# Performance work log

Measured on AMD Instinct MI355X. Metric: run time of the kernel, lower is better.

## Reference

```python
import jax, jax.numpy as jnp
import numpy as np

EPS = 1e-8
INV_SQRT = 1.0 / np.sqrt(1.0 + EPS)  # 1/sqrt(|k|+eps), |k|=1 for both hyp and sph


def layernorm(x, w, b, eps=1e-5):
    m = jnp.mean(x, axis=-1, keepdims=True)
    v = jnp.mean((x - m) ** 2, axis=-1, keepdims=True)
    return (x - m) * jax.lax.rsqrt(v + eps) * w + b


def setup_inputs() -> dict:
    key = jax.random.key(0)
    B, S, D, H = 4, 1024, 512, 8
    d = D // H
    FF = 2048
    ks = jax.random.split(key, 12)
    s_attn = 1.0 / np.sqrt(d)
    s_d = 1.0 / np.sqrt(D)
    s_ff = 1.0 / np.sqrt(FF)
    return {
        "x": jax.random.normal(ks[0], (B, S, D), jnp.float32),
        "Wq": jax.random.normal(ks[1], (H, d, d), jnp.float32) * s_attn,
        "Wk": jax.random.normal(ks[2], (H, d, d), jnp.float32) * s_attn,
        "Wv": jax.random.normal(ks[3], (H, d, d), jnp.float32) * s_attn,
        "gw": jnp.ones((H, 3), jnp.float32) / 3.0,
        "temp": jnp.ones((H,), jnp.float32),
        "Wo": jax.random.normal(ks[4], (D, D), jnp.float32) * s_d,
        "bo": jnp.zeros((D,), jnp.float32),
        "ln1_w": jnp.ones((D,), jnp.float32),
        "ln1_b": jnp.zeros((D,), jnp.float32),
        "ln2_w": jnp.ones((D,), jnp.float32),
        "ln2_b": jnp.zeros((D,), jnp.float32),
        "W1": jax.random.normal(ks[5], (FF, D), jnp.float32) * s_d,
        "b1": jnp.zeros((FF,), jnp.float32),
        "W2": jax.random.normal(ks[6], (D, FF), jnp.float32) * s_ff,
        "b2": jnp.zeros((D,), jnp.float32),
    }


def reference(x, Wq, Wk, Wv, gw, temp, Wo, bo, ln1_w, ln1_b, ln2_w, ln2_b, W1, b1, W2, b2):
    B, S, D = x.shape
    H = Wq.shape[0]
    d = D // H

    h = layernorm(x, ln1_w, ln1_b)
    xh = h.reshape(B, S, H, d).transpose(0, 2, 1, 3)  # [B,H,S,d]
    # nn.Linear: y = x @ W^T
    q = jnp.einsum("bhsd,hed->bhse", xh, Wq)
    k = jnp.einsum("bhsd,hed->bhse", xh, Wk)
    v = jnp.einsum("bhsd,hed->bhse", xh, Wv)

    qsq = jnp.sum(q * q, axis=-1)  # [B,H,S] == ||q||^2
    ksq = jnp.sum(k * k, axis=-1)
    qk = jnp.einsum("bhsd,bhtd->bhst", q, k)
    # ||q-k||^2 via expansion (same math as sum(diff^2), avoids [B,H,S,S,d])
    dsq = jnp.maximum(qsq[..., :, None] + ksq[..., None, :] - 2.0 * qk, 0.0)
    euc = jnp.sqrt(dsq + EPS)

    denom = (1.0 - qsq)[..., :, None] * (1.0 - ksq)[..., None, :] + EPS
    cosh_arg = jnp.clip(1.0 + 2.0 * dsq / denom, 1.0, 1e6)
    hyp = jnp.arccosh(cosh_arg) * INV_SQRT

    qn = jnp.sqrt(qsq)
    kn = jnp.sqrt(ksq)
    cos_angle = qk / ((qn + EPS)[..., :, None] * (kn + EPS)[..., None, :])
    cos_angle = jnp.clip(cos_angle, -1.0 + EPS, 1.0 - EPS)
    sph = jnp.arccos(cos_angle) * INV_SQRT

    w = jax.nn.softmax(gw, axis=-1)  # [H,3] per-head geometry mixing
    comb = (
        w[:, 0, None, None] * hyp
        + w[:, 1, None, None] * euc
        + w[:, 2, None, None] * sph
    )
    sim = -comb * temp[None, :, None, None]
    attn = jax.nn.softmax(sim, axis=-1)
    out = jnp.einsum("bhst,bhtd->bhsd", attn, v)
    out = out.transpose(0, 2, 1, 3).reshape(B, S, D)
    attn_out = out @ Wo.T + bo

    x = x + attn_out  # dropout=0 (eval)
    h2 = layernorm(x, ln2_w, ln2_b)
    ff = jax.nn.gelu(h2 @ W1.T + b1, approximate=False) @ W2.T + b2
    return x + ff, w
```

## Files before the change

### kernel.cpp

```cpp
#include <hip/hip_runtime.h>
#include <hip/hip_bf16.h>
#include <math.h>

typedef __attribute__((ext_vector_type(4))) float f32x4;
typedef __attribute__((ext_vector_type(8))) short bf16x8;
typedef unsigned short u16;
typedef unsigned int u32;

typedef f32x4  __attribute__((may_alias)) f32x4a;
typedef bf16x8 __attribute__((may_alias)) bf16x8a;
typedef uint2  __attribute__((may_alias)) uint2a;

__device__ __forceinline__ u16 bfbits(float f) {
  union { __hip_bfloat16 h; u16 u; } cv;
  cv.h = __float2bfloat16(f);
  return cv.u;
}
__device__ __forceinline__ float rcp_r(float x)  { return __builtin_amdgcn_rcpf(x); }
__device__ __forceinline__ float sqrt_r(float x) { return __builtin_amdgcn_sqrtf(x); }
__device__ __forceinline__ float log2_r(float x) { return __builtin_amdgcn_logf(x); }
__device__ __forceinline__ float exp2_r(float x) { return __builtin_amdgcn_exp2f(x); }
__device__ __forceinline__ u32 cvt_pk_bf16(float lo, float hi) {
  u32 r;
  asm("v_cvt_pk_bf16_f32 %0, %1, %2" : "=v"(r) : "v"(lo), "v"(hi));
  return r;
}
typedef const __attribute__((address_space(1))) unsigned int* gas_t;
typedef __attribute__((address_space(3))) unsigned int* las_t;
__device__ __forceinline__ void gload_lds16(const u16* g, u16* l) {
  __builtin_amdgcn_global_load_lds((gas_t)g, (las_t)l, 16, 0, 0);
}

__global__ __launch_bounds__(256) void convert_weights(
    const float* __restrict__ wq, const float* __restrict__ wk, const float* __restrict__ wv,
    const float* __restrict__ wo, const float* __restrict__ w1, const float* __restrict__ w2,
    u16* __restrict__ owq, u16* __restrict__ owk, u16* __restrict__ owv,
    u16* __restrict__ owo, u16* __restrict__ ow1, u16* __restrict__ ow2) {
  int i = blockIdx.x * 256 + threadIdx.x;
  const float* src; u16* dst; int base;
  if (i < 8192)        { src = wq; dst = owq; base = 0; }
  else if (i < 16384)  { src = wk; dst = owk; base = 8192; }
  else if (i < 24576)  { src = wv; dst = owv; base = 16384; }
  else if (i < 90112)  { src = wo; dst = owo; base = 24576; }
  else if (i < 352256) { src = w1; dst = ow1; base = 90112; }
  else                 { src = w2; dst = ow2; base = 352256; }
  int li = i - base;
  float4 v = reinterpret_cast<const float4*>(src)[li];
  ushort4 o;
  o.x = bfbits(v.x); o.y = bfbits(v.y); o.z = bfbits(v.z); o.w = bfbits(v.w);
  reinterpret_cast<ushort4*>(dst)[li] = o;
}

__global__ __launch_bounds__(128) void ln_kernel(const float* __restrict__ x,
    const float* __restrict__ w, const float* __restrict__ b, u16* __restrict__ out) {
  int row = blockIdx.x, tid = threadIdx.x;
  float4 v = reinterpret_cast<const float4*>(x + row * 512)[tid];
  float s  = v.x + v.y + v.z + v.w;
  float s2 = v.x*v.x + v.y*v.y + v.z*v.z + v.w*v.w;
  #pragma unroll
  for (int o = 32; o > 0; o >>= 1) { s += __shfl_down(s, o); s2 += __shfl_down(s2, o); }
  __shared__ float sm[4];
  if ((tid & 63) == 0) { sm[(tid >> 6)*2] = s; sm[(tid >> 6)*2 + 1] = s2; }
  __syncthreads();
  float ts = sm[0] + sm[2], ts2 = sm[1] + sm[3];
  float mean = ts * (1.f/512.f);
  float var  = ts2 * (1.f/512.f) - mean*mean;
  float rstd = __builtin_amdgcn_rsqf(var + 1e-5f);
  float4 wv = reinterpret_cast<const float4*>(w)[tid];
  float4 bv = reinterpret_cast<const float4*>(b)[tid];
  ushort4 o;
  o.x = bfbits((v.x-mean)*rstd*wv.x + bv.x);
  o.y = bfbits((v.y-mean)*rstd*wv.y + bv.y);
  o.z = bfbits((v.z-mean)*rstd*wv.z + bv.z);
  o.w = bfbits((v.w-mean)*rstd*wv.w + bv.w);
  reinterpret_cast<ushort4*>(out + row * 512)[tid] = o;
}

__global__ __launch_bounds__(256) void qkv_kernel(const u16* __restrict__ h1,
    const u16* __restrict__ wqb, const u16* __restrict__ wkb, const u16* __restrict__ wvb,
    u16* __restrict__ q, u16* __restrict__ k, u16* __restrict__ vt,
    float* __restrict__ qsq, float* __restrict__ ksq) {
  int mt = blockIdx.x, head = blockIdx.y;
  int wave = threadIdx.x >> 6, lane = threadIdx.x & 63;
  int lr = lane & 15, lg = lane >> 4;
  int m0 = mt * 64 + wave * 16;
  const u16* xr = h1 + (m0 + lr) * 512 + head * 64 + lg * 8;
  bf16x8 a0 = *reinterpret_cast<const bf16x8a*>(xr);
  bf16x8 a1 = *reinterpret_cast<const bf16x8a*>(xr + 32);
  int m_base = m0 + 4*lg;
  int bq = m_base >> 10;
  int s_base = m_base & 1023;
  int bh = (bq << 3) + head;
  #pragma unroll 1
  for (int mat = 0; mat < 3; ++mat) {
    const u16* W = (mat == 0 ? wqb : mat == 1 ? wkb : wvb) + head * 4096;
    f32x4 acc[4];
    #pragma unroll
    for (int c = 0; c < 4; c++)
      #pragma unroll
      for (int j = 0; j < 4; j++) acc[c][j] = 0.f;
    #pragma unroll
    for (int c = 0; c < 4; c++) {
      const u16* wr = W + (c*16 + lr) * 64 + lg * 8;
      bf16x8 b0 = *reinterpret_cast<const bf16x8a*>(wr);
      bf16x8 b1 = *reinterpret_cast<const bf16x8a*>(wr + 32);
      acc[c] = __builtin_amdgcn_mfma_f32_16x16x32_bf16(a0, b0, acc[c], 0, 0, 0);
      acc[c] = __builtin_amdgcn_mfma_f32_16x16x32_bf16(a1, b1, acc[c], 0, 0, 0);
    }
    if (mat == 2) {
      #pragma unroll
      for (int c = 0; c < 4; c++)
        #pragma unroll
        for (int j = 0; j < 4; j++)
          vt[(bh*64 + c*16 + lr) * 1024 + s_base + j] = bfbits(acc[c][j]);
    } else {
      u16* dst = (mat == 0 ? q : k);
      float* sq = (mat == 0 ? qsq : ksq);
      float ss[4] = {0.f, 0.f, 0.f, 0.f};
      #pragma unroll
      for (int c = 0; c < 4; c++)
        #pragma unroll
        for (int j = 0; j < 4; j++) {
          float vv = acc[c][j];
          dst[(bh*1024 + s_base + j) * 64 + c*16 + lr] = bfbits(vv);
          ss[j] += vv * vv;
        }
      #pragma unroll
      for (int j = 0; j < 4; j++) {
        #pragma unroll
        for (int o = 1; o < 16; o <<= 1) ss[j] += __shfl_xor(ss[j], o);
      }
      if (lr == 0) {
        #pragma unroll
        for (int j = 0; j < 4; j++) sq[bh*1024 + s_base + j] = ss[j];
      }
    }
  }
}

__global__ __launch_bounds__(512) void attn_kernel(
    const u16* __restrict__ q, const u16* __restrict__ k, const u16* __restrict__ vt,
    const float* __restrict__ qsqA, const float* __restrict__ ksqA,
    const float* __restrict__ gw, const float* __restrict__ temp,
    u16* __restrict__ attnb) {
  int bh = blockIdx.y;
  int b = bh >> 3, head = bh & 7;
  int tid = threadIdx.x;
  int wave = tid >> 6;
  int wq = wave & 1;
  int split = wave >> 1;
  int lane = tid & 63;
  int lr = lane & 15, lg = lane >> 4;
  int q0 = blockIdx.x * 32 + wq * 16;

  const u16* qp = q  + bh * 65536;
  const u16* kp = k  + bh * 65536;
  const u16* vp = vt + bh * 65536;

  __shared__ float ks_s[1024], rkn_s[1024];
  __shared__ __align__(16) char umem[32256];
  u16* pw = (u16*)umem + wave * 640;
  float* accR = (float*)umem;
  float* lR   = (float*)(umem + 30720);

  for (int i = tid; i < 1024; i += 512) {
    float kv = ksqA[bh * 1024 + i];
    ks_s[i] = kv;
    rkn_s[i] = rcp_r(sqrt_r(kv) + 1e-8f);
  }
  __syncthreads();

  float g0 = gw[head*3], g1 = gw[head*3+1], g2 = gw[head*3+2];
  float gm = fmaxf(g0, fmaxf(g1, g2));
  float e0 = __expf(g0-gm), e1 = __expf(g1-gm), e2 = __expf(g2-gm);
  float gi = rcp_r(e0 + e1 + e2);
  float tp = temp[head];
  const float LOG2E = 1.4426950408889634f;
  float chn = -e0*gi*tp;
  float cen = -e1*gi*tp*LOG2E;
  float csn = -e2*gi*tp*LOG2E;

  const u16* qr = qp + (q0 + lr) * 64 + lg * 8;
  bf16x8 aq0 = *reinterpret_cast<const bf16x8a*>(qr);
  bf16x8 aq1 = *reinterpret_cast<const bf16x8a*>(qr + 32);
  float qs  = qsqA[bh*1024 + q0 + lr];
  float omq = 1.f - qs;
  float rqn = rcp_r(sqrt_r(qs) + 1e-8f);

  f32x4 acc[4];
  #pragma unroll
  for (int c = 0; c < 4; c++)
    #pragma unroll
    for (int j = 0; j < 4; j++) acc[c][j] = 0.f;
  float psum0 = 0.f, psum1 = 0.f;

  for (int it = 0; it < 8; ++it) {
    int t0 = split * 256 + it * 32;
    const u16* kr = kp + (t0 + lr) * 64 + lg * 8;
    bf16x8 k00 = *reinterpret_cast<const bf16x8a*>(kr);
    bf16x8 k01 = *reinterpret_cast<const bf16x8a*>(kr + 32);
    bf16x8 k10 = *reinterpret_cast<const bf16x8a*>(kr + 1024);
    bf16x8 k11 = *reinterpret_cast<const bf16x8a*>(kr + 1024 + 32);
    f32x4 s0, s1;
    #pragma unroll
    for (int j = 0; j < 4; j++) { s0[j] = 0.f; s1[j] = 0.f; }
    s0 = __builtin_amdgcn_mfma_f32_16x16x32_bf16(k00, aq0, s0, 0, 0, 0);
    s0 = __builtin_amdgcn_mfma_f32_16x16x32_bf16(k01, aq1, s0, 0, 0, 0);
    s1 = __builtin_amdgcn_mfma_f32_16x16x32_bf16(k10, aq0, s1, 0, 0, 0);
    s1 = __builtin_amdgcn_mfma_f32_16x16x32_bf16(k11, aq1, s1, 0, 0, 0);

    f32x4 kq0 = *reinterpret_cast<const f32x4a*>(&ks_s[t0 + 4*lg]);
    f32x4 kq1 = *reinterpret_cast<const f32x4a*>(&ks_s[t0 + 16 + 4*lg]);
    f32x4 rk0 = *reinterpret_cast<const f32x4a*>(&rkn_s[t0 + 4*lg]);
    f32x4 rk1 = *reinterpret_cast<const f32x4a*>(&rkn_s[t0 + 16 + 4*lg]);

    float pv0[4], pv1[4];
    #pragma unroll
    for (int tc = 0; tc < 2; tc++) {
      f32x4 sv = tc ? s1 : s0;
      f32x4 kq = tc ? kq1 : kq0;
      f32x4 rk = tc ? rk1 : rk0;
      float* pv = tc ? pv1 : pv0;
      #pragma unroll
      for (int j = 0; j < 4; j++) {
        float qk  = sv[j];
        float ksj = kq[j];
        float dsq = fmaxf(fmaf(qk, -2.f, qs + ksj), 0.f);
        float euc = sqrt_r(dsq + 1e-8f);
        float den = fmaf(omq, 1.f - ksj, 1e-8f);
        float u   = (dsq + dsq) * rcp_r(den);
        u = fminf(fmaxf(u, 0.f), 999999.f);
        float hyp2 = log2_r((u + 1.f) + sqrt_r(u * (u + 2.f)));
        float ca = qk * rqn * rk[j];
        ca = fminf(fmaxf(ca, -1.f), 1.f);
        float aa = fabsf(ca);
        float pp = fmaf(aa, -0.0187293f, 0.0742610f);
        pp = fmaf(aa, pp, -0.2121144f);
        pp = fmaf(aa, pp, 1.5707288f);
        float rr = sqrt_r(1.f - aa) * pp;
        float sph = ca < 0.f ? 3.14159265358979f - rr : rr;
        float sim2 = fmaf(chn, hyp2, fmaf(cen, euc, csn * sph));
        float p = exp2_r(sim2);
        if (tc) psum1 += p; else psum0 += p;
        pv[j] = p;
      }
    }
    u32 w0 = cvt_pk_bf16(pv0[0], pv0[1]);
    u32 w1 = cvt_pk_bf16(pv0[2], pv0[3]);
    u32 w2 = cvt_pk_bf16(pv1[0], pv1[1]);
    u32 w3 = cvt_pk_bf16(pv1[2], pv1[3]);
    *reinterpret_cast<uint2a*>(pw + lr*40 + 4*lg)      = make_uint2(w0, w1);
    *reinterpret_cast<uint2a*>(pw + lr*40 + 16 + 4*lg) = make_uint2(w2, w3);
    bf16x8 pa = *reinterpret_cast<const bf16x8a*>(pw + lr*40 + lg*8);
    #pragma unroll
    for (int c = 0; c < 4; c++) {
      bf16x8 av = *reinterpret_cast<const bf16x8a*>(vp + (c*16 + lr)*1024 + t0 + lg*8);
      acc[c] = __builtin_amdgcn_mfma_f32_16x16x32_bf16(av, pa, acc[c], 0, 0, 0);
    }
  }

  float lt = psum0 + psum1;
  lt += __shfl_xor(lt, 16);
  lt += __shfl_xor(lt, 32);

  __syncthreads();
  if (split > 0) {
    int base = (wq*3 + split-1)*64 + lane;
    #pragma unroll
    for (int c = 0; c < 4; c++)
      *reinterpret_cast<f32x4a*>(accR + base*20 + c*4) = acc[c];
    lR[base] = lt;
  }
  __syncthreads();
  if (split == 0) {
    float ltot = lt;
    #pragma unroll
    for (int s = 0; s < 3; s++) ltot += lR[(wq*3+s)*64 + lane];
    float rl = rcp_r(ltot);
    #pragma unroll
    for (int c = 0; c < 4; c++) {
      f32x4 o = acc[c];
      #pragma unroll
      for (int s = 0; s < 3; s++)
        o += *reinterpret_cast<const f32x4a*>(accR + ((wq*3+s)*64+lane)*20 + c*4);
      ushort4 st;
      st.x = bfbits(o[0]*rl); st.y = bfbits(o[1]*rl);
      st.z = bfbits(o[2]*rl); st.w = bfbits(o[3]*rl);
      *reinterpret_cast<ushort4*>(
          &attnb[(size_t)((b << 10) + q0 + lr) * 512 + head*64 + c*16 + 4*lg]) = st;
    }
  }
}

template<int K, int BN, int MODE>
__global__ __launch_bounds__(256) void gemm_kernel(
    const u16* __restrict__ X, const u16* __restrict__ W,
    const float* __restrict__ bias, const float* __restrict__ res,
    float* __restrict__ outf, u16* __restrict__ outb,
    const float* __restrict__ gw, float* __restrict__ wout) {
  constexpr int NS = (MODE == 1) ? 2048 : 512;
  constexpr int BM = 128;
  constexpr int WM = (BN == 128) ? 64 : 32;
  constexpr int NFR = WM / 16;
  __shared__ u16 As[BM * 32];
  __shared__ u16 Bs[BN * 32];
  int tid = threadIdx.x;
  int wave = tid >> 6, lane = tid & 63;
  int lr = lane & 15, lg = lane >> 4;
  int wr = (BN == 128) ? (wave >> 1) : wave;
  int wc = (BN == 128) ? (wave & 1) : 0;
  int m0 = blockIdx.x * BM;
  int n0 = blockIdx.y * BN;
  f32x4 acc[NFR][4];
  #pragma unroll
  for (int fr = 0; fr < NFR; fr++)
    #pragma unroll
    for (int fc = 0; fc < 4; fc++)
      #pragma unroll
      for (int j = 0; j < 4; j++) acc[fr][fc][j] = 0.f;
  int chunk = wave * 64 + lane;
  int arow = chunk >> 2;
  int acol = ((chunk & 3) ^ (arow & 3)) << 3;
  const u16* Ag0 = X + (size_t)(m0 + arow) * K + acol;
  const u16* Ag1 = X + (size_t)(m0 + 64 + arow) * K + acol;
  const u16* Bg0 = W + (size_t)(n0 + arow) * K + acol;
  const u16* Bg1 = W + (size_t)(n0 + 64 + arow) * K + acol;
  u16* Al0 = As + wave * 512;
  u16* Al1 = As + 2048 + wave * 512;
  u16* Bl0 = Bs + wave * 512;
  u16* Bl1 = Bs + 2048 + wave * 512;
  int rdcol = ((lg ^ (lr & 3)) << 3);
  for (int k0 = 0; k0 < K; k0 += 32) {
    __syncthreads();
    gload_lds16(Ag0 + k0, Al0);
    gload_lds16(Ag1 + k0, Al1);
    gload_lds16(Bg0 + k0, Bl0);
    if constexpr (BN == 128) gload_lds16(Bg1 + k0, Bl1);
    __syncthreads();
    bf16x8 af[NFR], bfr[4];
    #pragma unroll
    for (int fr = 0; fr < NFR; fr++)
      af[fr] = *reinterpret_cast<const bf16x8a*>(As + (wr*WM + fr*16 + lr)*32 + rdcol);
    #pragma unroll
    for (int fc = 0; fc < 4; fc++)
      bfr[fc] = *reinterpret_cast<const bf16x8a*>(Bs + (wc*64 + fc*16 + lr)*32 + rdcol);
    #pragma unroll
    for (int fr = 0; fr < NFR; fr++)
      #pragma unroll
      for (int fc = 0; fc < 4; fc++)
        acc[fr][fc] = __builtin_amdgcn_mfma_f32_16x16x32_bf16(af[fr], bfr[fc], acc[fr][fc], 0, 0, 0);
  }
  #pragma unroll
  for (int fr = 0; fr < NFR; fr++)
    #pragma unroll
    for (int fc = 0; fc < 4; fc++) {
      int col = n0 + wc*64 + fc*16 + lr;
      float bb = bias[col];
      #pragma unroll
      for (int j = 0; j < 4; j++) {
        int row = m0 + wr*WM + fr*16 + 4*lg + j;
        float v = acc[fr][fc][j] + bb;
        if (MODE == 0 || MODE == 2) {
          outf[(size_t)row*NS + col] = v + res[(size_t)row*NS + col];
        } else {
          float t = v * fmaf(v*v, 0.035677408137f, 0.7978845608f);
          float g = v * rcp_r(1.f + exp2_r(-2.8853900817779268f * t));
          outb[(size_t)row*NS + col] = bfbits(g);
        }
      }
    }
  if (MODE == 2) {
    if (blockIdx.x == 0 && blockIdx.y == 0 && threadIdx.x < 8) {
      int h = threadIdx.x;
      float a0 = gw[h*3], a1 = gw[h*3+1], a2 = gw[h*3+2];
      float m = fmaxf(a0, fmaxf(a1, a2));
      float x0 = __expf(a0-m), x1 = __expf(a1-m), x2 = __expf(a2-m);
      float inv = rcp_r(x0 + x1 + x2);
      wout[h*3+0] = x0*inv; wout[h*3+1] = x1*inv; wout[h*3+2] = x2*inv;
    }
  }
}

extern "C" void kernel_launch(void* const* d_in, const int* in_sizes, int n_in,
                              void* d_out, int out_size, void* d_ws, size_t ws_size,
                              hipStream_t stream) {
  const float* x    = (const float*)d_in[0];
  const float* Wq   = (const float*)d_in[1];
  const float* Wk   = (const float*)d_in[2];
  const float* Wv   = (const float*)d_in[3];
  const float* gw   = (const float*)d_in[4];
  const float* temp = (const float*)d_in[5];
  const float* Wo   = (const float*)d_in[6];
  const float* bo   = (const float*)d_in[7];
  const float* ln1w = (const float*)d_in[8];
  const float* ln1b = (const float*)d_in[9];
  const float* ln2w = (const float*)d_in[10];
  const float* ln2b = (const float*)d_in[11];
  const float* W1   = (const float*)d_in[12];
  const float* b1   = (const float*)d_in[13];
  const float* W2   = (const float*)d_in[14];
  const float* b2   = (const float*)d_in[15];

  char* ws = (char*)d_ws;
  u16*  wqb  = (u16*)(ws + 0);
  u16*  wkb  = (u16*)(ws + 65536);
  u16*  wvb  = (u16*)(ws + 131072);
  u16*  wob  = (u16*)(ws + 196608);
  u16*  w1b  = (u16*)(ws + 720896);
  u16*  w2b  = (u16*)(ws + 2818048);
  u16*  h1b  = (u16*)(ws + 4915200);
  u16*  qb   = (u16*)(ws + 9109504);
  u16*  kb   = (u16*)(ws + 13303808);
  u16*  vtb  = (u16*)(ws + 17498112);
  float* qsq = (float*)(ws + 21692416);
  float* ksq = (float*)(ws + 21823488);
  u16*  attnb= (u16*)(ws + 21954560);
  float* x1  = (float*)(ws + 26148864);
  u16*  h2b  = (u16*)(ws + 34537472);
  u16*  gb   = (u16*)(ws + 4915200);

  float* outf = (float*)d_out;
  float* wout = outf + 4096*512;

  convert_weights<<<2400, 256, 0, stream>>>(Wq, Wk, Wv, Wo, W1, W2,
                                            wqb, wkb, wvb, wob, w1b, w2b);
  ln_kernel<<<4096, 128, 0, stream>>>(x, ln1w, ln1b, h1b);
  qkv_kernel<<<dim3(64, 8), 256, 0, stream>>>(h1b, wqb, wkb, wvb, qb, kb, vtb, qsq, ksq);
  attn_kernel<<<dim3(32, 32), 512, 0, stream>>>(qb, kb, vtb, qsq, ksq, gw, temp, attnb);
  gemm_kernel<512, 64, 0><<<dim3(32, 8), 256, 0, stream>>>(
      attnb, wob, bo, x, x1, nullptr, nullptr, nullptr);
  ln_kernel<<<4096, 128, 0, stream>>>(x1, ln2w, ln2b, h2b);
  gemm_kernel<512, 128, 1><<<dim3(32, 16), 256, 0, stream>>>(
      h2b, w1b, b1, nullptr, nullptr, gb, nullptr, nullptr);
  gemm_kernel<2048, 64, 2><<<dim3(32, 8), 256, 0, stream>>>(
      gb, w2b, b2, x1, outf, nullptr, gw, wout);
}
```

Before: 232.6 us.

## Precompute norm reciprocals, shrink attention blocks, split-K FF2 with combine kernel

The QKV kernel now also writes 1/(1-|v|^2) and rsqrt(|v|^2) for q and k, so attention reads these instead of computing reciprocals per score. Attention moves to 256-thread blocks with 16 queries each, twice as many blocks, no shared key-norm staging, and a serial cross-wave reduction. The GEMMs drop to 64-row tiles to launch more blocks, and FF2 is split along K into two partial outputs summed by a new combine kernel that also writes the softmax weights. This trades extra launches, partial-buffer traffic and more global loads of the norm arrays for higher occupancy and less per-element math. It also changes numerics: the small eps terms in the denominators are dropped.

```diff
diff --git a/kernel.cpp b/kernel.cpp
--- a/kernel.cpp
+++ b/kernel.cpp
@@ -20,6 +20,7 @@
 __device__ __forceinline__ float sqrt_r(float x) { return __builtin_amdgcn_sqrtf(x); }
 __device__ __forceinline__ float log2_r(float x) { return __builtin_amdgcn_logf(x); }
 __device__ __forceinline__ float exp2_r(float x) { return __builtin_amdgcn_exp2f(x); }
+__device__ __forceinline__ float rsq_r(float x)  { return __builtin_amdgcn_rsqf(x); }
 __device__ __forceinline__ u32 cvt_pk_bf16(float lo, float hi) {
   u32 r;
   asm("v_cvt_pk_bf16_f32 %0, %1, %2" : "=v"(r) : "v"(lo), "v"(hi));
@@ -65,7 +66,7 @@
   float ts = sm[0] + sm[2], ts2 = sm[1] + sm[3];
   float mean = ts * (1.f/512.f);
   float var  = ts2 * (1.f/512.f) - mean*mean;
-  float rstd = __builtin_amdgcn_rsqf(var + 1e-5f);
+  float rstd = rsq_r(var + 1e-5f);
   float4 wv = reinterpret_cast<const float4*>(w)[tid];
   float4 bv = reinterpret_cast<const float4*>(b)[tid];
   ushort4 o;
@@ -79,7 +80,8 @@
 __global__ __launch_bounds__(256) void qkv_kernel(const u16* __restrict__ h1,
     const u16* __restrict__ wqb, const u16* __restrict__ wkb, const u16* __restrict__ wvb,
     u16* __restrict__ q, u16* __restrict__ k, u16* __restrict__ vt,
-    float* __restrict__ qsq, float* __restrict__ ksq) {
+    float* __restrict__ qsq, float* __restrict__ qom, float* __restrict__ qrs,
+    float* __restrict__ ksq, float* __restrict__ kom, float* __restrict__ krs) {
   int mt = blockIdx.x, head = blockIdx.y;
   int wave = threadIdx.x >> 6, lane = threadIdx.x & 63;
   int lr = lane & 15, lg = lane >> 4;
@@ -116,6 +118,8 @@
     } else {
       u16* dst = (mat == 0 ? q : k);
       float* sq = (mat == 0 ? qsq : ksq);
+      float* om = (mat == 0 ? qom : kom);
+      float* rs = (mat == 0 ? qrs : krs);
       float ss[4] = {0.f, 0.f, 0.f, 0.f};
       #pragma unroll
       for (int c = 0; c < 4; c++)
@@ -132,43 +136,41 @@
       }
       if (lr == 0) {
         #pragma unroll
-        for (int j = 0; j < 4; j++) sq[bh*1024 + s_base + j] = ss[j];
+        for (int j = 0; j < 4; j++) {
+          float v = ss[j];
+          int idx = bh*1024 + s_base + j;
+          sq[idx] = v;
+          om[idx] = rcp_r(1.f - v);
+          rs[idx] = rsq_r(v);
+        }
       }
     }
   }
 }
 
-__global__ __launch_bounds__(512) void attn_kernel(
+__global__ __launch_bounds__(256, 8) void attn_kernel(
     const u16* __restrict__ q, const u16* __restrict__ k, const u16* __restrict__ vt,
-    const float* __restrict__ qsqA, const float* __restrict__ ksqA,
+    const float* __restrict__ qsqA, const float* __restrict__ qomA, const float* __restrict__ qrsA,
+    const float* __restrict__ ksqA, const float* __restrict__ komA, const float* __restrict__ krsA,
     const float* __restrict__ gw, const float* __restrict__ temp,
     u16* __restrict__ attnb) {
   int bh = blockIdx.y;
   int b = bh >> 3, head = bh & 7;
   int tid = threadIdx.x;
   int wave = tid >> 6;
-  int wq = wave & 1;
-  int split = wave >> 1;
   int lane = tid & 63;
   int lr = lane & 15, lg = lane >> 4;
-  int q0 = blockIdx.x * 32 + wq * 16;
+  int q0 = blockIdx.x * 16;
 
   const u16* qp = q  + bh * 65536;
   const u16* kp = k  + bh * 65536;
   const u16* vp = vt + bh * 65536;
-
-  __shared__ float ks_s[1024], rkn_s[1024];
-  __shared__ __align__(16) char umem[32256];
-  u16* pw = (u16*)umem + wave * 640;
-  float* accR = (float*)umem;
-  float* lR   = (float*)(umem + 30720);
-
-  for (int i = tid; i < 1024; i += 512) {
-    float kv = ksqA[bh * 1024 + i];
-    ks_s[i] = kv;
-    rkn_s[i] = rcp_r(sqrt_r(kv) + 1e-8f);
-  }
-  __syncthreads();
+  const float* ksb = ksqA + (bh << 10);
+  const float* kob = komA + (bh << 10);
+  const float* krb = krsA + (bh << 10);
+
+  __shared__ __align__(16) u16 umem[2560];
+  u16* pw = umem + wave * 640;
 
   float g0 = gw[head*3], g1 = gw[head*3+1], g2 = gw[head*3+2];
   float gm = fmaxf(g0, fmaxf(g1, g2));
@@ -183,9 +185,9 @@
   const u16* qr = qp + (q0 + lr) * 64 + lg * 8;
   bf16x8 aq0 = *reinterpret_cast<const bf16x8a*>(qr);
   bf16x8 aq1 = *reinterpret_cast<const bf16x8a*>(qr + 32);
-  float qs  = qsqA[bh*1024 + q0 + lr];
-  float omq = 1.f - qs;
-  float rqn = rcp_r(sqrt_r(qs) + 1e-8f);
+  float qs  = qsqA[(bh << 10) + q0 + lr];
+  float qom = qomA[(bh << 10) + q0 + lr];
+  float rqn = qrsA[(bh << 10) + q0 + lr];
 
   f32x4 acc[4];
   #pragma unroll
@@ -195,7 +197,7 @@
   float psum0 = 0.f, psum1 = 0.f;
 
   for (int it = 0; it < 8; ++it) {
-    int t0 = split * 256 + it * 32;
+    int t0 = wave * 256 + it * 32;
     const u16* kr = kp + (t0 + lr) * 64 + lg * 8;
     bf16x8 k00 = *reinterpret_cast<const bf16x8a*>(kr);
     bf16x8 k01 = *reinterpret_cast<const bf16x8a*>(kr + 32);
@@ -209,29 +211,24 @@
     s1 = __builtin_amdgcn_mfma_f32_16x16x32_bf16(k10, aq0, s1, 0, 0, 0);
     s1 = __builtin_amdgcn_mfma_f32_16x16x32_bf16(k11, aq1, s1, 0, 0, 0);
 
-    f32x4 kq0 = *reinterpret_cast<const f32x4a*>(&ks_s[t0 + 4*lg]);
-    f32x4 kq1 = *reinterpret_cast<const f32x4a*>(&ks_s[t0 + 16 + 4*lg]);
-    f32x4 rk0 = *reinterpret_cast<const f32x4a*>(&rkn_s[t0 + 4*lg]);
-    f32x4 rk1 = *reinterpret_cast<const f32x4a*>(&rkn_s[t0 + 16 + 4*lg]);
-
     float pv0[4], pv1[4];
     #pragma unroll
     for (int tc = 0; tc < 2; tc++) {
+      int tt = t0 + tc*16 + 4*lg;
+      f32x4 kq = *reinterpret_cast<const f32x4a*>(ksb + tt);
+      f32x4 ko = *reinterpret_cast<const f32x4a*>(kob + tt);
+      f32x4 krv = *reinterpret_cast<const f32x4a*>(krb + tt);
       f32x4 sv = tc ? s1 : s0;
-      f32x4 kq = tc ? kq1 : kq0;
-      f32x4 rk = tc ? rk1 : rk0;
       float* pv = tc ? pv1 : pv0;
       #pragma unroll
       for (int j = 0; j < 4; j++) {
         float qk  = sv[j];
-        float ksj = kq[j];
-        float dsq = fmaxf(fmaf(qk, -2.f, qs + ksj), 0.f);
+        float dsq = fmaxf(fmaf(qk, -2.f, qs + kq[j]), 0.f);
         float euc = sqrt_r(dsq + 1e-8f);
-        float den = fmaf(omq, 1.f - ksj, 1e-8f);
-        float u   = (dsq + dsq) * rcp_r(den);
+        float u   = (dsq + dsq) * qom * ko[j];
         u = fminf(fmaxf(u, 0.f), 999999.f);
         float hyp2 = log2_r((u + 1.f) + sqrt_r(u * (u + 2.f)));
-        float ca = qk * rqn * rk[j];
+        float ca = qk * rqn * krv[j];
         ca = fminf(fmaxf(ca, -1.f), 1.f);
         float aa = fabsf(ca);
         float pp = fmaf(aa, -0.0187293f, 0.0742610f);
@@ -263,121 +260,146 @@
   lt += __shfl_xor(lt, 16);
   lt += __shfl_xor(lt, 32);
 
+  float* fa = (float*)umem;
   __syncthreads();
-  if (split > 0) {
-    int base = (wq*3 + split-1)*64 + lane;
-    #pragma unroll
-    for (int c = 0; c < 4; c++)
-      *reinterpret_cast<f32x4a*>(accR + base*20 + c*4) = acc[c];
-    lR[base] = lt;
-  }
-  __syncthreads();
-  if (split == 0) {
-    float ltot = lt;
-    #pragma unroll
-    for (int s = 0; s < 3; s++) ltot += lR[(wq*3+s)*64 + lane];
-    float rl = rcp_r(ltot);
+  #pragma unroll 1
+  for (int s = 1; s <= 3; ++s) {
+    if (wave == s) {
+      #pragma unroll
+      for (int c = 0; c < 4; c++)
+        *reinterpret_cast<f32x4a*>(fa + lane*20 + c*4) = acc[c];
+      fa[lane*20 + 16] = lt;
+    }
+    __syncthreads();
+    if (wave == 0) {
+      #pragma unroll
+      for (int c = 0; c < 4; c++)
+        acc[c] += *reinterpret_cast<const f32x4a*>(fa + lane*20 + c*4);
+      lt += fa[lane*20 + 16];
+    }
+    __syncthreads();
+  }
+  if (wave == 0) {
+    float rl = rcp_r(lt);
     #pragma unroll
     for (int c = 0; c < 4; c++) {
-      f32x4 o = acc[c];
-      #pragma unroll
-      for (int s = 0; s < 3; s++)
-        o += *reinterpret_cast<const f32x4a*>(accR + ((wq*3+s)*64+lane)*20 + c*4);
       ushort4 st;
-      st.x = bfbits(o[0]*rl); st.y = bfbits(o[1]*rl);
-      st.z = bfbits(o[2]*rl); st.w = bfbits(o[3]*rl);
+      st.x = bfbits(acc[c][0]*rl); st.y = bfbits(acc[c][1]*rl);
+      st.z = bfbits(acc[c][2]*rl); st.w = bfbits(acc[c][3]*rl);
       *reinterpret_cast<ushort4*>(
           &attnb[(size_t)((b << 10) + q0 + lr) * 512 + head*64 + c*16 + 4*lg]) = st;
     }
   }
 }
 
-template<int K, int BN, int MODE>
-__global__ __launch_bounds__(256) void gemm_kernel(
+template<int K, int KS, int BN, int MODE>
+__global__ __launch_bounds__(256, 4) void gemm_kernel(
     const u16* __restrict__ X, const u16* __restrict__ W,
     const float* __restrict__ bias, const float* __restrict__ res,
-    float* __restrict__ outf, u16* __restrict__ outb,
+    float* __restrict__ outf, float* __restrict__ outf2, u16* __restrict__ outb,
     const float* __restrict__ gw, float* __restrict__ wout) {
   constexpr int NS = (MODE == 1) ? 2048 : 512;
-  constexpr int BM = 128;
-  constexpr int WM = (BN == 128) ? 64 : 32;
-  constexpr int NFR = WM / 16;
-  __shared__ u16 As[BM * 32];
+  constexpr int WN = BN / 2;
+  constexpr int NFC = WN / 16;
+  __shared__ u16 As[64 * 32];
   __shared__ u16 Bs[BN * 32];
   int tid = threadIdx.x;
   int wave = tid >> 6, lane = tid & 63;
   int lr = lane & 15, lg = lane >> 4;
-  int wr = (BN == 128) ? (wave >> 1) : wave;
-  int wc = (BN == 128) ? (wave & 1) : 0;
-  int m0 = blockIdx.x * BM;
-  int n0 = blockIdx.y * BN;
-  f32x4 acc[NFR][4];
+  int wr = wave >> 1, wc = wave & 1;
+  int m0 = blockIdx.x * 64, n0 = blockIdx.y * BN;
+  const u16* Xp = X;
+  const u16* Wp = W;
+  if constexpr (MODE == 3) { Xp += blockIdx.z * (KS/2); Wp += blockIdx.z * (KS/2); }
+  f32x4 acc[2][NFC];
   #pragma unroll
-  for (int fr = 0; fr < NFR; fr++)
-    #pragma unroll
-    for (int fc = 0; fc < 4; fc++)
+  for (int fr = 0; fr < 2; fr++)
+    #pragma unroll
+    for (int fc = 0; fc < NFC; fc++)
       #pragma unroll
       for (int j = 0; j < 4; j++) acc[fr][fc][j] = 0.f;
-  int chunk = wave * 64 + lane;
-  int arow = chunk >> 2;
-  int acol = ((chunk & 3) ^ (arow & 3)) << 3;
-  const u16* Ag0 = X + (size_t)(m0 + arow) * K + acol;
-  const u16* Ag1 = X + (size_t)(m0 + 64 + arow) * K + acol;
-  const u16* Bg0 = W + (size_t)(n0 + arow) * K + acol;
-  const u16* Bg1 = W + (size_t)(n0 + 64 + arow) * K + acol;
-  u16* Al0 = As + wave * 512;
-  u16* Al1 = As + 2048 + wave * 512;
+  int arow = tid >> 2;
+  int acol = ((tid & 3) ^ (arow & 3)) << 3;
+  const u16* Ag = Xp + (size_t)(m0 + arow) * KS + acol;
+  u16* Al = As + wave * 512;
+  const u16* Bg0 = Wp + (size_t)(n0 + arow) * KS + acol;
   u16* Bl0 = Bs + wave * 512;
-  u16* Bl1 = Bs + 2048 + wave * 512;
+  const u16* Bg1 = nullptr; u16* Bl1 = nullptr;
+  if constexpr (BN == 128) {
+    int c1 = 256 + tid, r1 = c1 >> 2;
+    int s1 = ((c1 & 3) ^ (r1 & 3)) << 3;
+    Bg1 = Wp + (size_t)(n0 + r1) * KS + s1;
+    Bl1 = Bs + 2048 + wave * 512;
+  }
   int rdcol = ((lg ^ (lr & 3)) << 3);
   for (int k0 = 0; k0 < K; k0 += 32) {
     __syncthreads();
-    gload_lds16(Ag0 + k0, Al0);
-    gload_lds16(Ag1 + k0, Al1);
-    gload_lds16(Bg0 + k0, Bl0);
+    gload_lds16(Ag + k0, Al);
+    if (BN != 32 || tid < 128) gload_lds16(Bg0 + k0, Bl0);
     if constexpr (BN == 128) gload_lds16(Bg1 + k0, Bl1);
     __syncthreads();
-    bf16x8 af[NFR], bfr[4];
-    #pragma unroll
-    for (int fr = 0; fr < NFR; fr++)
-      af[fr] = *reinterpret_cast<const bf16x8a*>(As + (wr*WM + fr*16 + lr)*32 + rdcol);
-    #pragma unroll
-    for (int fc = 0; fc < 4; fc++)
-      bfr[fc] = *reinterpret_cast<const bf16x8a*>(Bs + (wc*64 + fc*16 + lr)*32 + rdcol);
-    #pragma unroll
-    for (int fr = 0; fr < NFR; fr++)
-      #pragma unroll
-      for (int fc = 0; fc < 4; fc++)
+    bf16x8 af[2], bfr[NFC];
+    #pragma unroll
+    for (int fr = 0; fr < 2; fr++)
+      af[fr] = *reinterpret_cast<const bf16x8a*>(As + (wr*32 + fr*16 + lr)*32 + rdcol);
+    #pragma unroll
+    for (int fc = 0; fc < NFC; fc++)
+      bfr[fc] = *reinterpret_cast<const bf16x8a*>(Bs + (wc*WN + fc*16 + lr)*32 + rdcol);
+    #pragma unroll
+    for (int fr = 0; fr < 2; fr++)
+      #pragma unroll
+      for (int fc = 0; fc < NFC; fc++)
         acc[fr][fc] = __builtin_amdgcn_mfma_f32_16x16x32_bf16(af[fr], bfr[fc], acc[fr][fc], 0, 0, 0);
   }
+  float* po = nullptr;
+  if constexpr (MODE == 3) po = blockIdx.z ? outf2 : outf;
   #pragma unroll
-  for (int fr = 0; fr < NFR; fr++)
-    #pragma unroll
-    for (int fc = 0; fc < 4; fc++) {
-      int col = n0 + wc*64 + fc*16 + lr;
-      float bb = bias[col];
+  for (int fr = 0; fr < 2; fr++)
+    #pragma unroll
+    for (int fc = 0; fc < NFC; fc++) {
+      int col = n0 + wc*WN + fc*16 + lr;
+      float bb = (MODE == 3) ? 0.f : bias[col];
       #pragma unroll
       for (int j = 0; j < 4; j++) {
-        int row = m0 + wr*WM + fr*16 + 4*lg + j;
+        int row = m0 + wr*32 + fr*16 + 4*lg + j;
         float v = acc[fr][fc][j] + bb;
-        if (MODE == 0 || MODE == 2) {
+        if constexpr (MODE == 0) {
           outf[(size_t)row*NS + col] = v + res[(size_t)row*NS + col];
-        } else {
+        } else if constexpr (MODE == 1) {
           float t = v * fmaf(v*v, 0.035677408137f, 0.7978845608f);
           float g = v * rcp_r(1.f + exp2_r(-2.8853900817779268f * t));
           outb[(size_t)row*NS + col] = bfbits(g);
+        } else {
+          po[(size_t)row*512 + col] = v;
         }
       }
     }
-  if (MODE == 2) {
-    if (blockIdx.x == 0 && blockIdx.y == 0 && threadIdx.x < 8) {
-      int h = threadIdx.x;
-      float a0 = gw[h*3], a1 = gw[h*3+1], a2 = gw[h*3+2];
-      float m = fmaxf(a0, fmaxf(a1, a2));
-      float x0 = __expf(a0-m), x1 = __expf(a1-m), x2 = __expf(a2-m);
-      float inv = rcp_r(x0 + x1 + x2);
-      wout[h*3+0] = x0*inv; wout[h*3+1] = x1*inv; wout[h*3+2] = x2*inv;
-    }
+  (void)gw; (void)wout;
+}
+
+__global__ __launch_bounds__(256) void ff2_combine(
+    const float* __restrict__ p0, const float* __restrict__ p1,
+    const float* __restrict__ bias, const float* __restrict__ res,
+    float* __restrict__ out, const float* __restrict__ gw, float* __restrict__ wout) {
+  int i = blockIdx.x * 256 + threadIdx.x;
+  float4 a = reinterpret_cast<const float4*>(p0)[i];
+  float4 b = reinterpret_cast<const float4*>(p1)[i];
+  float4 r = reinterpret_cast<const float4*>(res)[i];
+  int col4 = (i & 127) << 2;
+  float4 bb = *reinterpret_cast<const float4*>(bias + col4);
+  float4 o;
+  o.x = a.x + b.x + r.x + bb.x;
+  o.y = a.y + b.y + r.y + bb.y;
+  o.z = a.z + b.z + r.z + bb.z;
+  o.w = a.w + b.w + r.w + bb.w;
+  reinterpret_cast<float4*>(out)[i] = o;
+  if (blockIdx.x == 0 && threadIdx.x < 8) {
+    int h = threadIdx.x;
+    float a0 = gw[h*3], a1 = gw[h*3+1], a2 = gw[h*3+2];
+    float m = fmaxf(a0, fmaxf(a1, a2));
+    float x0 = __expf(a0-m), x1 = __expf(a1-m), x2 = __expf(a2-m);
+    float inv = rcp_r(x0 + x1 + x2);
+    wout[h*3+0] = x0*inv; wout[h*3+1] = x1*inv; wout[h*3+2] = x2*inv;
   }
 }
 
@@ -414,9 +436,14 @@
   u16*  vtb  = (u16*)(ws + 17498112);
   float* qsq = (float*)(ws + 21692416);
   float* ksq = (float*)(ws + 21823488);
-  u16*  attnb= (u16*)(ws + 21954560);
-  float* x1  = (float*)(ws + 26148864);
-  u16*  h2b  = (u16*)(ws + 34537472);
+  float* qom = (float*)(ws + 21954560);
+  float* qrs = (float*)(ws + 22085632);
+  float* kom = (float*)(ws + 22216704);
+  float* krs = (float*)(ws + 22347776);
+  u16*  attnb= (u16*)(ws + 22478848);
+  float* x1  = (float*)(ws + 26673152);
+  u16*  h2b  = (u16*)(ws + 35061760);
+  float* p1f = (float*)(ws + 35061760);
   u16*  gb   = (u16*)(ws + 4915200);
 
   float* outf = (float*)d_out;
@@ -425,13 +452,16 @@
   convert_weights<<<2400, 256, 0, stream>>>(Wq, Wk, Wv, Wo, W1, W2,
                                             wqb, wkb, wvb, wob, w1b, w2b);
   ln_kernel<<<4096, 128, 0, stream>>>(x, ln1w, ln1b, h1b);
-  qkv_kernel<<<dim3(64, 8), 256, 0, stream>>>(h1b, wqb, wkb, wvb, qb, kb, vtb, qsq, ksq);
-  attn_kernel<<<dim3(32, 32), 512, 0, stream>>>(qb, kb, vtb, qsq, ksq, gw, temp, attnb);
-  gemm_kernel<512, 64, 0><<<dim3(32, 8), 256, 0, stream>>>(
-      attnb, wob, bo, x, x1, nullptr, nullptr, nullptr);
+  qkv_kernel<<<dim3(64, 8), 256, 0, stream>>>(h1b, wqb, wkb, wvb, qb, kb, vtb,
+                                              qsq, qom, qrs, ksq, kom, krs);
+  attn_kernel<<<dim3(64, 32), 256, 0, stream>>>(qb, kb, vtb, qsq, qom, qrs,
+                                                ksq, kom, krs, gw, temp, attnb);
+  gemm_kernel<512, 512, 32, 0><<<dim3(64, 16), 256, 0, stream>>>(
+      attnb, wob, bo, x, x1, nullptr, nullptr, nullptr, nullptr);
   ln_kernel<<<4096, 128, 0, stream>>>(x1, ln2w, ln2b, h2b);
-  gemm_kernel<512, 128, 1><<<dim3(32, 16), 256, 0, stream>>>(
-      h2b, w1b, b1, nullptr, nullptr, gb, nullptr, nullptr);
-  gemm_kernel<2048, 64, 2><<<dim3(32, 8), 256, 0, stream>>>(
-      gb, w2b, b2, x1, outf, nullptr, gw, wout);
-}
+  gemm_kernel<512, 512, 128, 1><<<dim3(64, 16), 256, 0, stream>>>(
+      h2b, w1b, b1, nullptr, nullptr, nullptr, gb, nullptr, nullptr);
+  gemm_kernel<1024, 2048, 64, 3><<<dim3(64, 8, 2), 256, 0, stream>>>(
+      gb, w2b, nullptr, nullptr, outf, p1f, nullptr, nullptr, nullptr);
+  ff2_combine<<<2048, 256, 0, stream>>>(outf, p1f, b2, x1, outf, gw, wout);
+}
```

Result: slower. 261.3 us (+12.3%).
